# Optimization experiments

Measured on AMD Instinct MI355X. Metric: run time of the kernel, lower is better.

The kernel has to match this reference:

```python
import jax, jax.numpy as jnp
import numpy as np

BN_EPS = 1e-5


def gcn_conv(x, src, dst, n, W, b):
    # PyG GCNConv: h = x @ W; add self-loops; symmetric deg^{-1/2} norm; scatter-add; + bias
    h = x @ W
    sl = jnp.arange(n, dtype=src.dtype)
    src_f = jnp.concatenate([src, sl])
    dst_f = jnp.concatenate([dst, sl])
    deg = jax.ops.segment_sum(jnp.ones_like(dst_f, dtype=h.dtype), dst_f, num_segments=n)
    dis = jnp.where(deg > 0, jax.lax.rsqrt(jnp.maximum(deg, 1.0)), 0.0)
    norm = dis[src_f] * dis[dst_f]                       # [E+N]
    msg = h[src_f] * norm[:, None]                       # gather + scale
    out = jax.ops.segment_sum(msg, dst_f, num_segments=n)  # scatter-add
    return out + b


def batchnorm(x, g, b):
    # training-mode BatchNorm1d (batch statistics), deterministic
    mu = jnp.mean(x, axis=0)
    var = jnp.mean((x - mu) ** 2, axis=0)
    return g * (x - mu) * jax.lax.rsqrt(var + BN_EPS) + b


def setup_inputs() -> dict:
    key = jax.random.key(0)
    ks = jax.random.split(key, 12)
    N, E, F_IN, D, M, G = 40000, 640000, 128, 128, 256, 2000
    x = jax.random.normal(ks[0], (N, F_IN), dtype=jnp.float32)
    edge_index = jax.random.randint(ks[1], (2, E), 0, N, dtype=jnp.int64)
    batch = jnp.sort(jax.random.randint(ks[2], (N,), 0, G, dtype=jnp.int64))
    s = lambda fi: 1.0 / np.sqrt(fi)
    W1 = jax.random.normal(ks[3], (F_IN, D), dtype=jnp.float32) * s(F_IN)
    b1 = jnp.zeros((D,), jnp.float32)
    W2 = jax.random.normal(ks[4], (D, D), dtype=jnp.float32) * s(D)
    b2 = jnp.zeros((D,), jnp.float32)
    bn1_g = jnp.ones((D,), jnp.float32); bn1_b = jnp.zeros((D,), jnp.float32)
    bn2_g = jnp.ones((D,), jnp.float32); bn2_b = jnp.zeros((D,), jnp.float32)
    fc1_w = jax.random.normal(ks[5], (D, M), dtype=jnp.float32) * s(D)
    fc1_b = jnp.zeros((M,), jnp.float32)
    fc2_w = jax.random.normal(ks[6], (M, M), dtype=jnp.float32) * s(M)
    fc2_b = jnp.zeros((M,), jnp.float32)
    fc3_w = jax.random.normal(ks[7], (M, 1), dtype=jnp.float32) * s(M)
    fc3_b = jnp.zeros((1,), jnp.float32)
    return dict(x=x, edge_index=edge_index, batch=batch, num_graphs=G,
                W1=W1, b1=b1, W2=W2, b2=b2,
                bn1_g=bn1_g, bn1_b=bn1_b, bn2_g=bn2_g, bn2_b=bn2_b,
                fc1_w=fc1_w, fc1_b=fc1_b, fc2_w=fc2_w, fc2_b=fc2_b,
                fc3_w=fc3_w, fc3_b=fc3_b)


def reference(x, edge_index, batch, num_graphs, W1, b1, W2, b2,
              bn1_g, bn1_b, bn2_g, bn2_b,
              fc1_w, fc1_b, fc2_w, fc2_b, fc3_w, fc3_b):
    n = x.shape[0]
    src, dst = edge_index[0], edge_index[1]
    h = gcn_conv(x, src, dst, n, W1, b1)
    h = jax.nn.relu(batchnorm(h, bn1_g, bn1_b))
    h = gcn_conv(h, src, dst, n, W2, b2)
    h = jax.nn.relu(batchnorm(h, bn2_g, bn2_b))
    g = jax.ops.segment_sum(h, batch, num_segments=num_graphs)  # scatter_sum pooling [G, D]
    g = jax.nn.relu(g @ fc1_w + fc1_b)   # dropout is identity in eval
    g = jax.nn.relu(g @ fc2_w + fc2_b)
    return g @ fc3_w + fc3_b             # [G, 1]
```

## Files before the change

kernel.cpp:

```cpp
#include <hip/hip_runtime.h>

#define NN 40000
#define NE 640000
#define DF 128
#define NG 2000
#define NCH 157

typedef unsigned int u32;
typedef __attribute__((ext_vector_type(8))) short short8;
typedef __attribute__((ext_vector_type(4))) float floatx4;

__device__ inline float2 bf2_to_f2(u32 u) {
    return make_float2(__uint_as_float(u << 16), __uint_as_float(u & 0xffff0000u));
}
__device__ inline u32 f_to_bf(float f) {
    u32 u = __float_as_uint(f);
    return (u + 0x7fffu + ((u >> 16) & 1u)) >> 16;
}
__device__ inline u32 pack_bf2(float a, float b) {
    return f_to_bf(a) | (f_to_bf(b) << 16);
}
__device__ inline float bf_to_f(short s) {
    return __uint_as_float(((u32)(unsigned short)s) << 16);
}

__global__ __launch_bounds__(256) void k_count(const int* __restrict__ dst, int* __restrict__ deg,
                                               const float* __restrict__ W1, const float* __restrict__ W2,
                                               unsigned short* __restrict__ wt1, unsigned short* __restrict__ wt2) {
    int bid = blockIdx.x;
    if (bid < NE / 256) {
        int e = bid * 256 + threadIdx.x;
        atomicAdd(&deg[dst[e]], 1);
        return;
    }
    const float* W = (bid == NE / 256) ? W1 : W2;
    unsigned short* wt = (bid == NE / 256) ? wt1 : wt2;
    for (int i = threadIdx.x; i < 128 * 128; i += 256) {
        int k = i >> 7, c = i & 127;
        wt[c * 128 + k] = (unsigned short)f_to_bf(W[i]);
    }
}

__global__ __launch_bounds__(256) void k_scan(const int* __restrict__ deg,
                                              int* __restrict__ row_ptr, int* __restrict__ cursor,
                                              float* __restrict__ dis) {
    __shared__ int red[256];
    __shared__ int ls[256];
    int tid = threadIdx.x;
    int blk = blockIdx.x;
    int limit = blk * 256;
    int partial = 0;
    for (int i = tid; i < limit; i += 256) partial += deg[i];
    red[tid] = partial;
    int i = limit + tid;
    int d = (i < NN) ? deg[i] : 0;
    ls[tid] = d;
    __syncthreads();
#pragma unroll
    for (int off = 128; off > 0; off >>= 1) {
        if (tid < off) red[tid] += red[tid + off];
        __syncthreads();
    }
    int base = red[0];
#pragma unroll
    for (int off = 1; off < 256; off <<= 1) {
        int t = (tid >= off) ? ls[tid - off] : 0;
        __syncthreads();
        ls[tid] += t;
        __syncthreads();
    }
    if (i < NN) {
        int r = base + ls[tid] - d;
        row_ptr[i] = r;
        cursor[i] = r;
        dis[i] = rsqrtf((float)(d + 1));
    }
    if (blk == NCH - 1 && tid == 0) row_ptr[NN] = NE;
}

template<bool BF16IN, bool FUSE_BN>
__device__ __forceinline__ void gemm_core(const void* __restrict__ Xv, const unsigned short* __restrict__ wt,
                                          u32* __restrict__ outb, const float* __restrict__ slots,
                                          const float* __restrict__ gam, const float* __restrict__ bet, int bid) {
    __shared__ unsigned short uni[128 * 136];
    __shared__ float sc[128], sh[128];
    unsigned short* wlds = uni;
    unsigned short* clds = uni;
    int tid = threadIdx.x;
    int row0 = bid * 128;

    if (FUSE_BN) {
        if (tid < 128) {
            float s = 0.f, q = 0.f;
            for (int k = 0; k < 64; k++) {
                s += slots[k * 256 + tid];
                q += slots[k * 256 + 128 + tid];
            }
            const float inv_n = 1.0f / (float)NN;
            float mu = s * inv_n;
            float va = fmaf(-mu, mu, q * inv_n);
            float a = gam[tid] * rsqrtf(va + 1e-5f);
            sc[tid] = a;
            sh[tid] = fmaf(-mu, a, bet[tid]);
        }
    }
    for (int i = tid; i < 2048; i += 256) {
        int c = i >> 4, s = i & 15;
        *(uint4*)&wlds[c * 136 + s * 8] = ((const uint4*)wt)[i];
    }
    __syncthreads();

    int lane = tid & 63;
    int wave = tid >> 6;
    int qr = lane >> 4;
    int rl = lane & 15;
    int rA0 = row0 + wave * 32 + rl;
    int rA1 = rA0 + 16;
    int rA0c = rA0 < NN ? rA0 : NN - 1;
    int rA1c = rA1 < NN ? rA1 : NN - 1;

    floatx4 acc[2][8];
#pragma unroll
    for (int a = 0; a < 2; a++)
#pragma unroll
        for (int b = 0; b < 8; b++) acc[a][b] = (floatx4){0.f, 0.f, 0.f, 0.f};

#pragma unroll
    for (int kb = 0; kb < 4; kb++) {
        int k0 = kb * 32 + qr * 8;
        short8 a0, a1;
        if (!BF16IN) {
            const float* p0 = (const float*)Xv + (size_t)rA0c * DF + k0;
            const float* p1 = (const float*)Xv + (size_t)rA1c * DF + k0;
            float4 u0 = *(const float4*)p0, u1 = *(const float4*)(p0 + 4);
            float4 v0 = *(const float4*)p1, v1 = *(const float4*)(p1 + 4);
            float fa[8] = {u0.x, u0.y, u0.z, u0.w, u1.x, u1.y, u1.z, u1.w};
            float fb[8] = {v0.x, v0.y, v0.z, v0.w, v1.x, v1.y, v1.z, v1.w};
#pragma unroll
            for (int j = 0; j < 8; j++) { a0[j] = (short)f_to_bf(fa[j]); a1[j] = (short)f_to_bf(fb[j]); }
        } else {
            a0 = *(const short8*)((const u32*)Xv + (size_t)rA0c * 64 + (k0 >> 1));
            a1 = *(const short8*)((const u32*)Xv + (size_t)rA1c * 64 + (k0 >> 1));
            if (FUSE_BN) {
                float4 s0 = *(const float4*)&sc[k0], s1 = *(const float4*)&sc[k0 + 4];
                float4 h0 = *(const float4*)&sh[k0], h1 = *(const float4*)&sh[k0 + 4];
                float ss[8] = {s0.x, s0.y, s0.z, s0.w, s1.x, s1.y, s1.z, s1.w};
                float hh[8] = {h0.x, h0.y, h0.z, h0.w, h1.x, h1.y, h1.z, h1.w};
#pragma unroll
                for (int j = 0; j < 8; j++) {
                    float f0 = fmaxf(fmaf(bf_to_f(a0[j]), ss[j], hh[j]), 0.f);
                    float f1 = fmaxf(fmaf(bf_to_f(a1[j]), ss[j], hh[j]), 0.f);
                    a0[j] = (short)f_to_bf(f0);
                    a1[j] = (short)f_to_bf(f1);
                }
            }
        }
#pragma unroll
        for (int ct = 0; ct < 8; ct++) {
            short8 bfr = *(const short8*)&wlds[(ct * 16 + rl) * 136 + k0];
            acc[0][ct] = __builtin_amdgcn_mfma_f32_16x16x32_bf16(a0, bfr, acc[0][ct], 0, 0, 0);
            acc[1][ct] = __builtin_amdgcn_mfma_f32_16x16x32_bf16(a1, bfr, acc[1][ct], 0, 0, 0);
        }
    }
    __syncthreads();
#pragma unroll
    for (int rt = 0; rt < 2; rt++)
#pragma unroll
        for (int ct = 0; ct < 8; ct++)
#pragma unroll
            for (int r = 0; r < 4; r++) {
                int lr = wave * 32 + rt * 16 + qr * 4 + r;
                int c = ct * 16 + rl;
                clds[lr * 136 + c] = (unsigned short)f_to_bf(acc[rt][ct][r]);
            }
    __syncthreads();
    for (int i = tid; i < 2048; i += 256) {
        int lr = i >> 4, s = i & 15;
        int grow = row0 + lr;
        if (grow < NN) {
            uint4 v = *(const uint4*)&clds[lr * 136 + s * 8];
            ((uint4*)(outb + (size_t)grow * 64))[s] = v;
        }
    }
}

__global__ __launch_bounds__(256, 4) void k_fillgemm(const int* __restrict__ src, const int* __restrict__ dst,
                                                     int* __restrict__ cursor, int* __restrict__ col,
                                                     const float* __restrict__ X, const unsigned short* __restrict__ wt1,
                                                     u32* __restrict__ outb) {
    if (blockIdx.x < NE / 256) {
        int e = blockIdx.x * 256 + threadIdx.x;
        int p = atomicAdd(&cursor[dst[e]], 1);
        col[p] = src[e];
        return;
    }
    gemm_core<false, false>(X, wt1, outb, nullptr, nullptr, nullptr, blockIdx.x - NE / 256);
}

__global__ __launch_bounds__(256, 4) void k_gemm2(const u32* __restrict__ Hb, const unsigned short* __restrict__ wt2,
                                                  u32* __restrict__ outb, const float* __restrict__ slots,
                                                  const float* __restrict__ gam, const float* __restrict__ bet) {
    gemm_core<true, true>(Hb, wt2, outb, slots, gam, bet, blockIdx.x);
}

__global__ __launch_bounds__(256) void k_gather(const u32* __restrict__ Hb, const int* __restrict__ row_ptr,
                                                const int* __restrict__ col, const float* __restrict__ dis,
                                                const float* __restrict__ bias, u32* __restrict__ outb,
                                                float* __restrict__ slots) {
    __shared__ float sred[4][128];
    __shared__ float qred[4][128];
    int t = threadIdx.x & 63;
    int wv = threadIdx.x >> 6;
    int node = blockIdx.x * 4 + wv;
    float di = dis[node];
    float2 acc;
    {
        float2 a = bf2_to_f2(Hb[(size_t)node * 64 + t]);
        float s = di * di;
        acc = make_float2(a.x * s, a.y * s);
    }
    int lo = row_ptr[node], hi = row_ptr[node + 1];
    for (int base = lo; base < hi; base += 64) {
        int m = hi - base; if (m > 64) m = 64;
        int sidx = 0; float sw = 0.f;
        if (t < m) { sidx = col[base + t]; sw = di * dis[sidx]; }
        int j = 0;
        for (; j + 8 <= m; j += 8) {
            int s0 = __shfl(sidx, j),     s1 = __shfl(sidx, j + 1);
            int s2 = __shfl(sidx, j + 2), s3 = __shfl(sidx, j + 3);
            int s4 = __shfl(sidx, j + 4), s5 = __shfl(sidx, j + 5);
            int s6 = __shfl(sidx, j + 6), s7 = __shfl(sidx, j + 7);
            float w0 = __shfl(sw, j),     w1 = __shfl(sw, j + 1);
            float w2 = __shfl(sw, j + 2), w3 = __shfl(sw, j + 3);
            float w4 = __shfl(sw, j + 4), w5 = __shfl(sw, j + 5);
            float w6 = __shfl(sw, j + 6), w7 = __shfl(sw, j + 7);
            u32 u0 = Hb[(size_t)s0 * 64 + t], u1 = Hb[(size_t)s1 * 64 + t];
            u32 u2 = Hb[(size_t)s2 * 64 + t], u3 = Hb[(size_t)s3 * 64 + t];
            u32 u4 = Hb[(size_t)s4 * 64 + t], u5 = Hb[(size_t)s5 * 64 + t];
            u32 u6 = Hb[(size_t)s6 * 64 + t], u7 = Hb[(size_t)s7 * 64 + t];
            float2 h0 = bf2_to_f2(u0), h1 = bf2_to_f2(u1), h2 = bf2_to_f2(u2), h3 = bf2_to_f2(u3);
            float2 h4 = bf2_to_f2(u4), h5 = bf2_to_f2(u5), h6 = bf2_to_f2(u6), h7 = bf2_to_f2(u7);
            acc.x = fmaf(h3.x, w3, fmaf(h2.x, w2, fmaf(h1.x, w1, fmaf(h0.x, w0, acc.x))));
            acc.y = fmaf(h3.y, w3, fmaf(h2.y, w2, fmaf(h1.y, w1, fmaf(h0.y, w0, acc.y))));
            acc.x = fmaf(h7.x, w7, fmaf(h6.x, w6, fmaf(h5.x, w5, fmaf(h4.x, w4, acc.x))));
            acc.y = fmaf(h7.y, w7, fmaf(h6.y, w6, fmaf(h5.y, w5, fmaf(h4.y, w4, acc.y))));
        }
        for (; j < m; j++) {
            int s0 = __shfl(sidx, j); float w0 = __shfl(sw, j);
            float2 h0 = bf2_to_f2(Hb[(size_t)s0 * 64 + t]);
            acc.x = fmaf(h0.x, w0, acc.x);
            acc.y = fmaf(h0.y, w0, acc.y);
        }
    }
    float2 b = ((const float2*)bias)[t];
    acc.x += b.x; acc.y += b.y;
    outb[(size_t)node * 64 + t] = pack_bf2(acc.x, acc.y);
    sred[wv][2 * t] = acc.x;     sred[wv][2 * t + 1] = acc.y;
    qred[wv][2 * t] = acc.x * acc.x; qred[wv][2 * t + 1] = acc.y * acc.y;
    __syncthreads();
    int tid = threadIdx.x;
    if (tid < 128) {
        float s = sred[0][tid] + sred[1][tid] + sred[2][tid] + sred[3][tid];
        float q = qred[0][tid] + qred[1][tid] + qred[2][tid] + qred[3][tid];
        int slot = blockIdx.x & 63;
        atomicAdd(&slots[slot * 256 + tid], s);
        atomicAdd(&slots[slot * 256 + 128 + tid], q);
    }
}

__global__ __launch_bounds__(256) void k_poolfc(const u32* __restrict__ Hb, const int* __restrict__ batch,
                                                const float* __restrict__ slots,
                                                const float* __restrict__ gam, const float* __restrict__ bet,
                                                const float* __restrict__ fc1w, const float* __restrict__ fc1b,
                                                const float* __restrict__ fc2w, const float* __restrict__ fc2b,
                                                const float* __restrict__ fc3w, const float* __restrict__ fc3b,
                                                float* __restrict__ out) {
    __shared__ float sc[128], sh[128];
    __shared__ float pooled[4][128];
    __shared__ float g1[4][256];
    __shared__ float g2[4][256];
    __shared__ int bnds[5];
    int tid = threadIdx.x;
    int gbase = blockIdx.x * 4;
    if (tid < 128) {
        float s = 0.f, q = 0.f;
        for (int k = 0; k < 64; k++) {
            s += slots[k * 256 + tid];
            q += slots[k * 256 + 128 + tid];
        }
        const float inv_n = 1.0f / (float)NN;
        float mu = s * inv_n;
        float va = fmaf(-mu, mu, q * inv_n);
        float a = gam[tid] * rsqrtf(va + 1e-5f);
        sc[tid] = a;
        sh[tid] = fmaf(-mu, a, bet[tid]);
    } else if (tid < 133) {
        int target = gbase + (tid - 128);
        int a = 0, b = NN;
        while (a < b) { int m = (a + b) >> 1; if (batch[m] < target) a = m + 1; else b = m; }
        bnds[tid - 128] = a;
    }
    __syncthreads();
    {
        int g = tid >> 6, p = tid & 63;
        int lo = bnds[g], hi = bnds[g + 1];
        float a0 = 0.f, a1 = 0.f;
        float sc0 = sc[2 * p], sh0 = sh[2 * p], sc1 = sc[2 * p + 1], sh1 = sh[2 * p + 1];
        for (int i = lo; i < hi; i++) {
            float2 v = bf2_to_f2(Hb[(size_t)i * 64 + p]);
            a0 += fmaxf(fmaf(v.x, sc0, sh0), 0.f);
            a1 += fmaxf(fmaf(v.y, sc1, sh1), 0.f);
        }
        pooled[g][2 * p] = a0;
        pooled[g][2 * p + 1] = a1;
    }
    __syncthreads();
    {
        float x0 = 0.f, x1 = 0.f, x2 = 0.f, x3 = 0.f;
        for (int k = 0; k < 128; k++) {
            float wv = fc1w[k * 256 + tid];
            x0 = fmaf(pooled[0][k], wv, x0);
            x1 = fmaf(pooled[1][k], wv, x1);
            x2 = fmaf(pooled[2][k], wv, x2);
            x3 = fmaf(pooled[3][k], wv, x3);
        }
        float bb = fc1b[tid];
        g1[0][tid] = fmaxf(x0 + bb, 0.f);
        g1[1][tid] = fmaxf(x1 + bb, 0.f);
        g1[2][tid] = fmaxf(x2 + bb, 0.f);
        g1[3][tid] = fmaxf(x3 + bb, 0.f);
    }
    __syncthreads();
    {
        float x0 = 0.f, x1 = 0.f, x2 = 0.f, x3 = 0.f;
        for (int k = 0; k < 256; k++) {
            float wv = fc2w[k * 256 + tid];
            x0 = fmaf(g1[0][k], wv, x0);
            x1 = fmaf(g1[1][k], wv, x1);
            x2 = fmaf(g1[2][k], wv, x2);
            x3 = fmaf(g1[3][k], wv, x3);
        }
        float bb = fc2b[tid];
        g2[0][tid] = fmaxf(x0 + bb, 0.f);
        g2[1][tid] = fmaxf(x1 + bb, 0.f);
        g2[2][tid] = fmaxf(x2 + bb, 0.f);
        g2[3][tid] = fmaxf(x3 + bb, 0.f);
    }
    __syncthreads();
    {
        int lane = tid & 63, wv = tid >> 6;
        float s = fmaf(g2[wv][lane], fc3w[lane],
                  fmaf(g2[wv][64 + lane], fc3w[64 + lane],
                  fmaf(g2[wv][128 + lane], fc3w[128 + lane],
                       g2[wv][192 + lane] * fc3w[192 + lane])));
        for (int off = 32; off > 0; off >>= 1) s += __shfl_down(s, off);
        if (lane == 0) out[gbase + wv] = s + fc3b[0];
    }
}

extern "C" void kernel_launch(void* const* d_in, const int* in_sizes, int n_in,
                              void* d_out, int out_size, void* d_ws, size_t ws_size,
                              hipStream_t stream) {
    const float* x    = (const float*)d_in[0];
    const int*   ei   = (const int*)d_in[1];
    const int*   batch= (const int*)d_in[2];
    const float* W1   = (const float*)d_in[4];
    const float* b1   = (const float*)d_in[5];
    const float* W2   = (const float*)d_in[6];
    const float* b2   = (const float*)d_in[7];
    const float* bn1g = (const float*)d_in[8];
    const float* bn1b = (const float*)d_in[9];
    const float* bn2g = (const float*)d_in[10];
    const float* bn2b = (const float*)d_in[11];
    const float* fc1w = (const float*)d_in[12];
    const float* fc1b = (const float*)d_in[13];
    const float* fc2w = (const float*)d_in[14];
    const float* fc2b = (const float*)d_in[15];
    const float* fc3w = (const float*)d_in[16];
    const float* fc3b = (const float*)d_in[17];
    const int* src = ei;
    const int* dst = ei + NE;
    float* outp = (float*)d_out;

    char* w = (char*)d_ws;
    size_t o = 0;
    auto alloc = [&](size_t bytes) -> char* {
        char* p = w + o;
        o = (o + bytes + 255) & ~(size_t)255;
        return p;
    };
    int*   deg     = (int*)alloc((size_t)NN * 4);
    float* slotsA  = (float*)alloc(64 * 256 * 4);
    float* slotsB  = (float*)alloc(64 * 256 * 4);
    char*  zend    = w + o;
    int*   row_ptr = (int*)alloc((size_t)(NN + 1) * 4);
    int*   cursor  = (int*)alloc((size_t)NN * 4);
    int*   col     = (int*)alloc((size_t)NE * 4);
    float* dis     = (float*)alloc((size_t)NN * 4);
    unsigned short* wt1 = (unsigned short*)alloc(128 * 128 * 2);
    unsigned short* wt2 = (unsigned short*)alloc(128 * 128 * 2);
    u32*   bufA    = (u32*)alloc((size_t)NN * 64 * 4);
    u32*   bufB    = (u32*)alloc((size_t)NN * 64 * 4);

    hipMemsetAsync(deg, 0, (size_t)(zend - (char*)deg), stream);

    const int GEMM_BLKS = (NN + 127) / 128;
    k_count<<<NE / 256 + 2, 256, 0, stream>>>(dst, deg, W1, W2, wt1, wt2);
    k_scan<<<NCH, 256, 0, stream>>>(deg, row_ptr, cursor, dis);
    k_fillgemm<<<NE / 256 + GEMM_BLKS, 256, 0, stream>>>(src, dst, cursor, col, x, wt1, bufA);
    k_gather<<<NN / 4, 256, 0, stream>>>(bufA, row_ptr, col, dis, b1, bufB, slotsA);
    k_gemm2<<<GEMM_BLKS, 256, 0, stream>>>(bufB, wt2, bufA, slotsA, bn1g, bn1b);
    k_gather<<<NN / 4, 256, 0, stream>>>(bufA, row_ptr, col, dis, b2, bufB, slotsB);
    k_poolfc<<<NG / 4, 256, 0, stream>>>(bufB, batch, slotsB, bn2g, bn2b,
                                         fc1w, fc1b, fc2w, fc2b, fc3w, fc3b, outp);
}
```

Measured before the change: 306.2 us.

## Move first GEMM into degree-count kernel and batch four edges per thread

The first-layer GEMM moves from the fill kernel into the degree-count kernel. Each GEMM block now converts and transposes W1 from fp32 straight into LDS, so the separate wt1 pass is gone. The count and fill kernels now handle four edges per thread with independent atomics, using 625 blocks instead of 2500. The aim is to overlap the dense GEMM with the atomic degree counting and give the atomics more memory-level parallelism. The cost is that every one of the 313 GEMM blocks repeats the fp32 W1 conversion, with strided scalar LDS writes.

```diff
diff --git a/kernel.cpp b/kernel.cpp
--- a/kernel.cpp
+++ b/kernel.cpp
@@ -5,6 +5,8 @@
 #define DF 128
 #define NG 2000
 #define NCH 157
+#define FILLB 625
+#define GEMM_BLKS 313
 
 typedef unsigned int u32;
 typedef __attribute__((ext_vector_type(8))) short short8;
@@ -24,21 +26,143 @@
     return __uint_as_float(((u32)(unsigned short)s) << 16);
 }
 
-__global__ __launch_bounds__(256) void k_count(const int* __restrict__ dst, int* __restrict__ deg,
-                                               const float* __restrict__ W1, const float* __restrict__ W2,
-                                               unsigned short* __restrict__ wt1, unsigned short* __restrict__ wt2) {
+template<bool BF16IN, bool FUSE_BN, bool WT_F32>
+__device__ __forceinline__ void gemm_core(const void* __restrict__ Xv, const void* __restrict__ wsrc,
+                                          u32* __restrict__ outb, const float* __restrict__ slots,
+                                          const float* __restrict__ gam, const float* __restrict__ bet, int bid) {
+    __shared__ unsigned short uni[128 * 136];
+    __shared__ float sc[128], sh[128];
+    unsigned short* wlds = uni;
+    unsigned short* clds = uni;
+    int tid = threadIdx.x;
+    int row0 = bid * 128;
+
+    if (FUSE_BN) {
+        if (tid < 128) {
+            float s = 0.f, q = 0.f;
+            for (int k = 0; k < 64; k++) {
+                s += slots[k * 256 + tid];
+                q += slots[k * 256 + 128 + tid];
+            }
+            const float inv_n = 1.0f / (float)NN;
+            float mu = s * inv_n;
+            float va = fmaf(-mu, mu, q * inv_n);
+            float a = gam[tid] * rsqrtf(va + 1e-5f);
+            sc[tid] = a;
+            sh[tid] = fmaf(-mu, a, bet[tid]);
+        }
+    }
+    if (WT_F32) {
+        const float* W = (const float*)wsrc;
+        for (int i = tid; i < 16384; i += 256) {
+            int k = i >> 7, c = i & 127;
+            wlds[c * 136 + k] = (unsigned short)f_to_bf(W[i]);
+        }
+    } else {
+        const unsigned short* wt = (const unsigned short*)wsrc;
+        for (int i = tid; i < 2048; i += 256) {
+            int c = i >> 4, s = i & 15;
+            *(uint4*)&wlds[c * 136 + s * 8] = ((const uint4*)wt)[i];
+        }
+    }
+    __syncthreads();
+
+    int lane = tid & 63;
+    int wave = tid >> 6;
+    int qr = lane >> 4;
+    int rl = lane & 15;
+    int rA0 = row0 + wave * 32 + rl;
+    int rA1 = rA0 + 16;
+    int rA0c = rA0 < NN ? rA0 : NN - 1;
+    int rA1c = rA1 < NN ? rA1 : NN - 1;
+
+    floatx4 acc[2][8];
+#pragma unroll
+    for (int a = 0; a < 2; a++)
+#pragma unroll
+        for (int b = 0; b < 8; b++) acc[a][b] = (floatx4){0.f, 0.f, 0.f, 0.f};
+
+#pragma unroll
+    for (int kb = 0; kb < 4; kb++) {
+        int k0 = kb * 32 + qr * 8;
+        short8 a0, a1;
+        if (!BF16IN) {
+            const float* p0 = (const float*)Xv + (size_t)rA0c * DF + k0;
+            const float* p1 = (const float*)Xv + (size_t)rA1c * DF + k0;
+            float4 u0 = *(const float4*)p0, u1 = *(const float4*)(p0 + 4);
+            float4 v0 = *(const float4*)p1, v1 = *(const float4*)(p1 + 4);
+            float fa[8] = {u0.x, u0.y, u0.z, u0.w, u1.x, u1.y, u1.z, u1.w};
+            float fb[8] = {v0.x, v0.y, v0.z, v0.w, v1.x, v1.y, v1.z, v1.w};
+#pragma unroll
+            for (int j = 0; j < 8; j++) { a0[j] = (short)f_to_bf(fa[j]); a1[j] = (short)f_to_bf(fb[j]); }
+        } else {
+            a0 = *(const short8*)((const u32*)Xv + (size_t)rA0c * 64 + (k0 >> 1));
+            a1 = *(const short8*)((const u32*)Xv + (size_t)rA1c * 64 + (k0 >> 1));
+            if (FUSE_BN) {
+                float4 s0 = *(const float4*)&sc[k0], s1 = *(const float4*)&sc[k0 + 4];
+                float4 h0 = *(const float4*)&sh[k0], h1 = *(const float4*)&sh[k0 + 4];
+                float ss[8] = {s0.x, s0.y, s0.z, s0.w, s1.x, s1.y, s1.z, s1.w};
+                float hh[8] = {h0.x, h0.y, h0.z, h0.w, h1.x, h1.y, h1.z, h1.w};
+#pragma unroll
+                for (int j = 0; j < 8; j++) {
+                    float f0 = fmaxf(fmaf(bf_to_f(a0[j]), ss[j], hh[j]), 0.f);
+                    float f1 = fmaxf(fmaf(bf_to_f(a1[j]), ss[j], hh[j]), 0.f);
+                    a0[j] = (short)f_to_bf(f0);
+                    a1[j] = (short)f_to_bf(f1);
+                }
+            }
+        }
+#pragma unroll
+        for (int ct = 0; ct < 8; ct++) {
+            short8 bfr = *(const short8*)&wlds[(ct * 16 + rl) * 136 + k0];
+            acc[0][ct] = __builtin_amdgcn_mfma_f32_16x16x32_bf16(a0, bfr, acc[0][ct], 0, 0, 0);
+            acc[1][ct] = __builtin_amdgcn_mfma_f32_16x16x32_bf16(a1, bfr, acc[1][ct], 0, 0, 0);
+        }
+    }
+    __syncthreads();
+#pragma unroll
+    for (int rt = 0; rt < 2; rt++)
+#pragma unroll
+        for (int ct = 0; ct < 8; ct++)
+#pragma unroll
+            for (int r = 0; r < 4; r++) {
+                int lr = wave * 32 + rt * 16 + qr * 4 + r;
+                int c = ct * 16 + rl;
+                clds[lr * 136 + c] = (unsigned short)f_to_bf(acc[rt][ct][r]);
+            }
+    __syncthreads();
+    for (int i = tid; i < 2048; i += 256) {
+        int lr = i >> 4, s = i & 15;
+        int grow = row0 + lr;
+        if (grow < NN) {
+            uint4 v = *(const uint4*)&clds[lr * 136 + s * 8];
+            ((uint4*)(outb + (size_t)grow * 64))[s] = v;
+        }
+    }
+}
+
+__global__ __launch_bounds__(256, 4) void k_countgemm(const int* __restrict__ dst, int* __restrict__ deg,
+                                                      const float* __restrict__ W1, const float* __restrict__ W2,
+                                                      unsigned short* __restrict__ wt2,
+                                                      const float* __restrict__ X, u32* __restrict__ outb) {
     int bid = blockIdx.x;
-    if (bid < NE / 256) {
-        int e = bid * 256 + threadIdx.x;
-        atomicAdd(&deg[dst[e]], 1);
+    if (bid < FILLB) {
+        int e0 = bid * 1024 + threadIdx.x;
+        int d0 = dst[e0], d1 = dst[e0 + 256], d2 = dst[e0 + 512], d3 = dst[e0 + 768];
+        atomicAdd(&deg[d0], 1);
+        atomicAdd(&deg[d1], 1);
+        atomicAdd(&deg[d2], 1);
+        atomicAdd(&deg[d3], 1);
         return;
     }
-    const float* W = (bid == NE / 256) ? W1 : W2;
-    unsigned short* wt = (bid == NE / 256) ? wt1 : wt2;
-    for (int i = threadIdx.x; i < 128 * 128; i += 256) {
-        int k = i >> 7, c = i & 127;
-        wt[c * 128 + k] = (unsigned short)f_to_bf(W[i]);
-    }
+    if (bid == FILLB) {
+        for (int i = threadIdx.x; i < 128 * 128; i += 256) {
+            int k = i >> 7, c = i & 127;
+            wt2[c * 128 + k] = (unsigned short)f_to_bf(W2[i]);
+        }
+        return;
+    }
+    gemm_core<false, false, true>(X, W1, outb, nullptr, nullptr, nullptr, bid - FILLB - 1);
 }
 
 __global__ __launch_bounds__(256) void k_scan(const int* __restrict__ deg,
@@ -78,129 +202,25 @@
     if (blk == NCH - 1 && tid == 0) row_ptr[NN] = NE;
 }
 
-template<bool BF16IN, bool FUSE_BN>
-__device__ __forceinline__ void gemm_core(const void* __restrict__ Xv, const unsigned short* __restrict__ wt,
-                                          u32* __restrict__ outb, const float* __restrict__ slots,
-                                          const float* __restrict__ gam, const float* __restrict__ bet, int bid) {
-    __shared__ unsigned short uni[128 * 136];
-    __shared__ float sc[128], sh[128];
-    unsigned short* wlds = uni;
-    unsigned short* clds = uni;
-    int tid = threadIdx.x;
-    int row0 = bid * 128;
-
-    if (FUSE_BN) {
-        if (tid < 128) {
-            float s = 0.f, q = 0.f;
-            for (int k = 0; k < 64; k++) {
-                s += slots[k * 256 + tid];
-                q += slots[k * 256 + 128 + tid];
-            }
-            const float inv_n = 1.0f / (float)NN;
-            float mu = s * inv_n;
-            float va = fmaf(-mu, mu, q * inv_n);
-            float a = gam[tid] * rsqrtf(va + 1e-5f);
-            sc[tid] = a;
-            sh[tid] = fmaf(-mu, a, bet[tid]);
-        }
-    }
-    for (int i = tid; i < 2048; i += 256) {
-        int c = i >> 4, s = i & 15;
-        *(uint4*)&wlds[c * 136 + s * 8] = ((const uint4*)wt)[i];
-    }
-    __syncthreads();
-
-    int lane = tid & 63;
-    int wave = tid >> 6;
-    int qr = lane >> 4;
-    int rl = lane & 15;
-    int rA0 = row0 + wave * 32 + rl;
-    int rA1 = rA0 + 16;
-    int rA0c = rA0 < NN ? rA0 : NN - 1;
-    int rA1c = rA1 < NN ? rA1 : NN - 1;
-
-    floatx4 acc[2][8];
-#pragma unroll
-    for (int a = 0; a < 2; a++)
-#pragma unroll
-        for (int b = 0; b < 8; b++) acc[a][b] = (floatx4){0.f, 0.f, 0.f, 0.f};
-
-#pragma unroll
-    for (int kb = 0; kb < 4; kb++) {
-        int k0 = kb * 32 + qr * 8;
-        short8 a0, a1;
-        if (!BF16IN) {
-            const float* p0 = (const float*)Xv + (size_t)rA0c * DF + k0;
-            const float* p1 = (const float*)Xv + (size_t)rA1c * DF + k0;
-            float4 u0 = *(const float4*)p0, u1 = *(const float4*)(p0 + 4);
-            float4 v0 = *(const float4*)p1, v1 = *(const float4*)(p1 + 4);
-            float fa[8] = {u0.x, u0.y, u0.z, u0.w, u1.x, u1.y, u1.z, u1.w};
-            float fb[8] = {v0.x, v0.y, v0.z, v0.w, v1.x, v1.y, v1.z, v1.w};
-#pragma unroll
-            for (int j = 0; j < 8; j++) { a0[j] = (short)f_to_bf(fa[j]); a1[j] = (short)f_to_bf(fb[j]); }
-        } else {
-            a0 = *(const short8*)((const u32*)Xv + (size_t)rA0c * 64 + (k0 >> 1));
-            a1 = *(const short8*)((const u32*)Xv + (size_t)rA1c * 64 + (k0 >> 1));
-            if (FUSE_BN) {
-                float4 s0 = *(const float4*)&sc[k0], s1 = *(const float4*)&sc[k0 + 4];
-                float4 h0 = *(const float4*)&sh[k0], h1 = *(const float4*)&sh[k0 + 4];
-                float ss[8] = {s0.x, s0.y, s0.z, s0.w, s1.x, s1.y, s1.z, s1.w};
-                float hh[8] = {h0.x, h0.y, h0.z, h0.w, h1.x, h1.y, h1.z, h1.w};
-#pragma unroll
-                for (int j = 0; j < 8; j++) {
-                    float f0 = fmaxf(fmaf(bf_to_f(a0[j]), ss[j], hh[j]), 0.f);
-                    float f1 = fmaxf(fmaf(bf_to_f(a1[j]), ss[j], hh[j]), 0.f);
-                    a0[j] = (short)f_to_bf(f0);
-                    a1[j] = (short)f_to_bf(f1);
-                }
-            }
-        }
-#pragma unroll
-        for (int ct = 0; ct < 8; ct++) {
-            short8 bfr = *(const short8*)&wlds[(ct * 16 + rl) * 136 + k0];
-            acc[0][ct] = __builtin_amdgcn_mfma_f32_16x16x32_bf16(a0, bfr, acc[0][ct], 0, 0, 0);
-            acc[1][ct] = __builtin_amdgcn_mfma_f32_16x16x32_bf16(a1, bfr, acc[1][ct], 0, 0, 0);
-        }
-    }
-    __syncthreads();
-#pragma unroll
-    for (int rt = 0; rt < 2; rt++)
-#pragma unroll
-        for (int ct = 0; ct < 8; ct++)
-#pragma unroll
-            for (int r = 0; r < 4; r++) {
-                int lr = wave * 32 + rt * 16 + qr * 4 + r;
-                int c = ct * 16 + rl;
-                clds[lr * 136 + c] = (unsigned short)f_to_bf(acc[rt][ct][r]);
-            }
-    __syncthreads();
-    for (int i = tid; i < 2048; i += 256) {
-        int lr = i >> 4, s = i & 15;
-        int grow = row0 + lr;
-        if (grow < NN) {
-            uint4 v = *(const uint4*)&clds[lr * 136 + s * 8];
-            ((uint4*)(outb + (size_t)grow * 64))[s] = v;
-        }
-    }
-}
-
-__global__ __launch_bounds__(256, 4) void k_fillgemm(const int* __restrict__ src, const int* __restrict__ dst,
-                                                     int* __restrict__ cursor, int* __restrict__ col,
-                                                     const float* __restrict__ X, const unsigned short* __restrict__ wt1,
-                                                     u32* __restrict__ outb) {
-    if (blockIdx.x < NE / 256) {
-        int e = blockIdx.x * 256 + threadIdx.x;
-        int p = atomicAdd(&cursor[dst[e]], 1);
-        col[p] = src[e];
-        return;
-    }
-    gemm_core<false, false>(X, wt1, outb, nullptr, nullptr, nullptr, blockIdx.x - NE / 256);
+__global__ __launch_bounds__(256) void k_fill(const int* __restrict__ src, const int* __restrict__ dst,
+                                              int* __restrict__ cursor, int* __restrict__ col) {
+    int e0 = blockIdx.x * 1024 + threadIdx.x;
+    int d0 = dst[e0], d1 = dst[e0 + 256], d2 = dst[e0 + 512], d3 = dst[e0 + 768];
+    int s0 = src[e0], s1 = src[e0 + 256], s2 = src[e0 + 512], s3 = src[e0 + 768];
+    int p0 = atomicAdd(&cursor[d0], 1);
+    int p1 = atomicAdd(&cursor[d1], 1);
+    int p2 = atomicAdd(&cursor[d2], 1);
+    int p3 = atomicAdd(&cursor[d3], 1);
+    col[p0] = s0;
+    col[p1] = s1;
+    col[p2] = s2;
+    col[p3] = s3;
 }
 
 __global__ __launch_bounds__(256, 4) void k_gemm2(const u32* __restrict__ Hb, const unsigned short* __restrict__ wt2,
                                                   u32* __restrict__ outb, const float* __restrict__ slots,
                                                   const float* __restrict__ gam, const float* __restrict__ bet) {
-    gemm_core<true, true>(Hb, wt2, outb, slots, gam, bet, blockIdx.x);
+    gemm_core<true, true, false>(Hb, wt2, outb, slots, gam, bet, blockIdx.x);
 }
 
 __global__ __launch_bounds__(256) void k_gather(const u32* __restrict__ Hb, const int* __restrict__ row_ptr,
@@ -397,17 +417,15 @@
     int*   cursor  = (int*)alloc((size_t)NN * 4);
     int*   col     = (int*)alloc((size_t)NE * 4);
     float* dis     = (float*)alloc((size_t)NN * 4);
-    unsigned short* wt1 = (unsigned short*)alloc(128 * 128 * 2);
     unsigned short* wt2 = (unsigned short*)alloc(128 * 128 * 2);
     u32*   bufA    = (u32*)alloc((size_t)NN * 64 * 4);
     u32*   bufB    = (u32*)alloc((size_t)NN * 64 * 4);
 
     hipMemsetAsync(deg, 0, (size_t)(zend - (char*)deg), stream);
 
-    const int GEMM_BLKS = (NN + 127) / 128;
-    k_count<<<NE / 256 + 2, 256, 0, stream>>>(dst, deg, W1, W2, wt1, wt2);
+    k_countgemm<<<FILLB + 1 + GEMM_BLKS, 256, 0, stream>>>(dst, deg, W1, W2, wt2, x, bufA);
     k_scan<<<NCH, 256, 0, stream>>>(deg, row_ptr, cursor, dis);
-    k_fillgemm<<<NE / 256 + GEMM_BLKS, 256, 0, stream>>>(src, dst, cursor, col, x, wt1, bufA);
+    k_fill<<<FILLB, 256, 0, stream>>>(src, dst, cursor, col);
     k_gather<<<NN / 4, 256, 0, stream>>>(bufA, row_ptr, col, dis, b1, bufB, slotsA);
     k_gemm2<<<GEMM_BLKS, 256, 0, stream>>>(bufB, wt2, bufA, slotsA, bn1g, bn1b);
     k_gather<<<NN / 4, 256, 0, stream>>>(bufA, row_ptr, col, dis, b2, bufB, slotsB);
```

After: 299.6 us. 2.2% less time.
